# Kernel tuning notes

Measured on AMD Instinct MI355X. Metric: run time of the kernel, lower is better.

The kernel has to match this reference:

```python
import jax, jax.numpy as jnp
import numpy as np
from jax import lax

T, B, H = 8192, 16, 256
D0, D1, D2 = 64, 64, 128


def setup_inputs() -> dict:
    key = jax.random.key(0)
    ks = jax.random.split(key, 16)
    k = 1.0 / np.sqrt(H)  # torch LSTMCell default init scale

    def u(kk, shape):
        return jax.random.uniform(kk, shape, jnp.float32, -k, k)

    inp = {
        "x0": jax.random.normal(ks[0], (T, B, D0), jnp.float32),
        "x1": jax.random.normal(ks[1], (T // 2, B, D1), jnp.float32),
        "x2": jax.random.normal(ks[2], (T // 4, B, D2), jnp.float32),
    }
    # one LSTMCell per possible concatenated input size: a=256 (all), b=128 (two), c=64 (one)
    sizes = [("a", D0 + D1 + D2), ("b", D0 + D1), ("c", D0)]
    i = 3
    for name, s in sizes:
        inp[f"W_ih_{name}"] = u(ks[i], (4 * H, s)); i += 1
        inp[f"W_hh_{name}"] = u(ks[i], (4 * H, H)); i += 1
        inp[f"b_ih_{name}"] = u(ks[i], (4 * H,)); i += 1
        inp[f"b_hh_{name}"] = u(ks[i], (4 * H,)); i += 1
    return inp


def _cell(x, h, c, Wih, Whh, bih, bhh):
    # torch.nn.LSTMCell: gates = x W_ih^T + b_ih + h W_hh^T + b_hh; order i,f,g,o
    g = x @ Wih.T + bih + h @ Whh.T + bhh
    i, f, gg, o = jnp.split(g, 4, axis=-1)
    c2 = jax.nn.sigmoid(f) * c + jax.nn.sigmoid(i) * jnp.tanh(gg)
    h2 = jax.nn.sigmoid(o) * jnp.tanh(c2)
    return h2, c2


def reference(x0, x1, x2,
              W_ih_a, W_hh_a, b_ih_a, b_hh_a,
              W_ih_b, W_hh_b, b_ih_b, b_hh_b,
              W_ih_c, W_hh_c, b_ih_c, b_hh_c):
    # ratios = [1, 2, 4]; active sets are nested: t%4==0 -> all 3, t%2==0 -> first 2, else first only
    def step(carry, t):
        h, c = carry

        def br_all(_):
            xt = jnp.concatenate([x0[t], x1[t // 2], x2[t // 4]], axis=-1)  # [B, 256]
            return _cell(xt, h, c, W_ih_a, W_hh_a, b_ih_a, b_hh_a)

        def br_two(_):
            xt = jnp.concatenate([x0[t], x1[t // 2]], axis=-1)  # [B, 128]
            return _cell(xt, h, c, W_ih_b, W_hh_b, b_ih_b, b_hh_b)

        def br_one(_):
            return _cell(x0[t], h, c, W_ih_c, W_hh_c, b_ih_c, b_hh_c)  # [B, 64]

        branch = jnp.where(t % 4 == 0, 0, jnp.where(t % 2 == 0, 1, 2))
        h2, c2 = lax.switch(branch, [br_all, br_two, br_one], None)
        return (h2, c2), h2

    h0 = jnp.zeros((B, H), jnp.float32)
    (_, _), ys = lax.scan(step, (h0, h0), jnp.arange(T))
    return ys  # [T, B, H]
```

## Files before the change

### kernel.cpp

```cpp
#include <hip/hip_runtime.h>
#include <stdint.h>


typedef _Float16 half8 __attribute__((ext_vector_type(8)));
typedef float floatx4 __attribute__((ext_vector_type(4)));
typedef unsigned int u32x4 __attribute__((ext_vector_type(4)));

#define T_STEPS 8192
#define NWG 16

__device__ __forceinline__ float fsig(float x) {
    return __builtin_amdgcn_rcpf(1.0f + __expf(-x));
}
__device__ __forceinline__ float ftanh(float x) {
    return 1.0f - 2.0f * __builtin_amdgcn_rcpf(1.0f + __expf(2.0f * x));
}

__device__ __forceinline__ half8 ld8w(const float* p) {
    floatx4 a = *(const floatx4*)p;
    floatx4 b = *(const floatx4*)(p + 4);
    half8 h;
    h[0] = (_Float16)a[0]; h[1] = (_Float16)a[1]; h[2] = (_Float16)a[2]; h[3] = (_Float16)a[3];
    h[4] = (_Float16)b[0]; h[5] = (_Float16)b[1]; h[6] = (_Float16)b[2]; h[7] = (_Float16)b[3];
    return h;
}

__device__ __forceinline__ void ld64_sc1(const void* p, u32x4& a, u32x4& b, u32x4& c, u32x4& d) {
    asm volatile(
        "global_load_dwordx4 %0, %4, off sc1\n\t"
        "global_load_dwordx4 %1, %4, off offset:16 sc1\n\t"
        "global_load_dwordx4 %2, %4, off offset:32 sc1\n\t"
        "global_load_dwordx4 %3, %4, off offset:48 sc1\n\t"
        "s_waitcnt vmcnt(0)"
        : "=&v"(a), "=&v"(b), "=&v"(c), "=&v"(d)
        : "v"(p)
        : "memory");
}
__device__ __forceinline__ void st16_sc1(void* p, u32x4 v) {
    asm volatile("global_store_dwordx4 %0, %1, off sc1" :: "v"(p), "v"(v) : "memory");
}

__global__ __launch_bounds__(256, 1) void lstm_kernel(
    const float* __restrict__ x0, const float* __restrict__ x1, const float* __restrict__ x2,
    const float* __restrict__ Wih_a, const float* __restrict__ Whh_a,
    const float* __restrict__ bih_a, const float* __restrict__ bhh_a,
    const float* __restrict__ Wih_b, const float* __restrict__ Whh_b,
    const float* __restrict__ bih_b, const float* __restrict__ bhh_b,
    const float* __restrict__ Wih_c, const float* __restrict__ Whh_c,
    const float* __restrict__ bih_c, const float* __restrict__ bhh_c,
    float* __restrict__ out, uint8_t* __restrict__ ws, int smask)
{
    const int tid = threadIdx.x;
    const int g   = blockIdx.x;
    const int w   = tid >> 6;
    const int l   = tid & 63;
    const int n   = l & 15;
    const int mg  = l >> 4;
    const int up  = n & 3;
    const int gt  = n >> 2;
    const int unit = g * 16 + w * 4 + up;
    const int R    = gt * 256 + unit;

    uint8_t* hring = ws;

    __shared__ _Float16 XH[16][520];

    half8 wfa[16], wfb[12], wfc[10];
    {
        const int ko = mg * 8;
        #pragma unroll
        for (int kt = 0; kt < 8; ++kt) wfa[kt]     = ld8w(Wih_a + (size_t)R * 256 + kt * 32 + ko);
        #pragma unroll
        for (int kt = 0; kt < 8; ++kt) wfa[8 + kt] = ld8w(Whh_a + (size_t)R * 256 + kt * 32 + ko);
        #pragma unroll
        for (int kt = 0; kt < 4; ++kt) wfb[kt]     = ld8w(Wih_b + (size_t)R * 128 + kt * 32 + ko);
        #pragma unroll
        for (int kt = 0; kt < 8; ++kt) wfb[4 + kt] = ld8w(Whh_b + (size_t)R * 256 + kt * 32 + ko);
        #pragma unroll
        for (int kt = 0; kt < 2; ++kt) wfc[kt]     = ld8w(Wih_c + (size_t)R * 64  + kt * 32 + ko);
        #pragma unroll
        for (int kt = 0; kt < 8; ++kt) wfc[2 + kt] = ld8w(Whh_c + (size_t)R * 256 + kt * 32 + ko);
    }
    const float ba = bih_a[R] + bhh_a[R];
    const float bb = bih_b[R] + bhh_b[R];
    const float bc = bih_c[R] + bhh_c[R];

    float cst[4] = {0.f, 0.f, 0.f, 0.f};

    for (int t = 0; t < T_STEPS; ++t) {
        __syncthreads();

        const int br = ((t & 3) == 0) ? 0 : (((t & 1) == 0) ? 1 : 2);
        const int kx = (br == 0) ? 256 : ((br == 1) ? 128 : 64);

        if (tid < 128) {
            const int m = tid >> 3, cg = (tid & 7) * 8;
            *(half8*)&XH[m][cg] = ld8w(x0 + (size_t)t * 1024 + m * 64 + cg);
        } else if (br < 2) {
            const int tt = tid - 128;
            const int m = tt >> 3, cg = (tt & 7) * 8;
            *(half8*)&XH[m][64 + cg] = ld8w(x1 + (size_t)(t >> 1) * 1024 + m * 64 + cg);
        }
        if (br == 0) {
            const int m = tid >> 4, cg = (tid & 15) * 8;
            *(half8*)&XH[m][128 + cg] = ld8w(x2 + (size_t)(t >> 2) * 2048 + m * 128 + cg);
        }

        {
            const int row = tid >> 4, u = tid & 15;
            _Float16* dst = &XH[row][kx + u * 16];
            if (t == 0) {
                *(u32x4*)dst       = (u32x4)0u;
                *(u32x4*)(dst + 8) = (u32x4)0u;
            } else {
                const uint32_t want = (uint32_t)(t - 1);
                const uint8_t* src = hring + (size_t)((t - 1) & smask) * 16384
                                   + (size_t)row * 1024 + (size_t)u * 64;
                u32x4 a, b, c, d;
                for (;;) {
                    ld64_sc1(src, a, b, c, d);
                    if (a[1] == want && a[3] == want && b[1] == want && b[3] == want &&
                        c[1] == want && c[3] == want && d[1] == want && d[3] == want)
                        break;
                }
                u32x4 lo = {a[0], a[2], b[0], b[2]};
                u32x4 hi = {c[0], c[2], d[0], d[2]};
                *(u32x4*)dst       = lo;
                *(u32x4*)(dst + 8) = hi;
            }
        }
        __syncthreads();

        floatx4 ac0 = {0.f, 0.f, 0.f, 0.f}, ac1 = {0.f, 0.f, 0.f, 0.f};
        {
            const int ao = mg * 8;
            if (br == 0) {
                #pragma unroll
                for (int kt = 0; kt < 16; kt += 2) {
                    ac0 = __builtin_amdgcn_mfma_f32_16x16x32_f16(
                        *(const half8*)&XH[n][kt * 32 + ao], wfa[kt], ac0, 0, 0, 0);
                    ac1 = __builtin_amdgcn_mfma_f32_16x16x32_f16(
                        *(const half8*)&XH[n][(kt + 1) * 32 + ao], wfa[kt + 1], ac1, 0, 0, 0);
                }
            } else if (br == 1) {
                #pragma unroll
                for (int kt = 0; kt < 12; kt += 2) {
                    ac0 = __builtin_amdgcn_mfma_f32_16x16x32_f16(
                        *(const half8*)&XH[n][kt * 32 + ao], wfb[kt], ac0, 0, 0, 0);
                    ac1 = __builtin_amdgcn_mfma_f32_16x16x32_f16(
                        *(const half8*)&XH[n][(kt + 1) * 32 + ao], wfb[kt + 1], ac1, 0, 0, 0);
                }
            } else {
                #pragma unroll
                for (int kt = 0; kt < 10; kt += 2) {
                    ac0 = __builtin_amdgcn_mfma_f32_16x16x32_f16(
                        *(const half8*)&XH[n][kt * 32 + ao], wfc[kt], ac0, 0, 0, 0);
                    ac1 = __builtin_amdgcn_mfma_f32_16x16x32_f16(
                        *(const half8*)&XH[n][(kt + 1) * 32 + ao], wfc[kt + 1], ac1, 0, 0, 0);
                }
            }
        }
        const floatx4 acc = ac0 + ac1;

        const float bsel = (br == 0) ? ba : ((br == 1) ? bb : bc);
        float tv[4];
        #pragma unroll
        for (int r = 0; r < 4; ++r) {
            const float gv = acc[r] + bsel;
            tv[r] = (gt == 2) ? ftanh(gv) : fsig(gv);
        }
        float h2v[4];
        const int b0 = l & ~12;
        #pragma unroll
        for (int r = 0; r < 4; ++r) {
            const float vi = __shfl(tv[r], b0,      64);
            const float vf = __shfl(tv[r], b0 + 4,  64);
            const float vg = __shfl(tv[r], b0 + 8,  64);
            const float vo = __shfl(tv[r], b0 + 12, 64);
            const float c2 = vf * cst[r] + vi * vg;
            cst[r] = c2;
            h2v[r] = vo * ftanh(c2);
        }

        {
            uint8_t* sb = hring + (size_t)(t & smask) * 16384 + (size_t)(8 * g + 2 * w) * 8;
            const int s0 = l & ~15;
            #pragma unroll
            for (int r = 0; r < 4; ++r) {
                const unsigned hv =
                    (unsigned)__builtin_bit_cast(unsigned short, (_Float16)h2v[r]);
                const unsigned v0 = (unsigned)__shfl((int)hv, s0,     64);
                const unsigned v1 = (unsigned)__shfl((int)hv, s0 + 1, 64);
                const unsigned v2 = (unsigned)__shfl((int)hv, s0 + 2, 64);
                const unsigned v3 = (unsigned)__shfl((int)hv, s0 + 3, 64);
                if (n == 0) {
                    u32x4 pk = { (v0 & 0xffffu) | (v1 << 16), (unsigned)t,
                                 (v2 & 0xffffu) | (v3 << 16), (unsigned)t };
                    st16_sc1(sb + (size_t)(mg * 4 + r) * 1024, pk);
                }
            }
        }

        if (gt == 0) {
            float* op = out + (size_t)t * 4096 + (size_t)(mg * 4) * 256 + unit;
            #pragma unroll
            for (int r = 0; r < 4; ++r) op[r * 256] = h2v[r];
        }
    }
}

extern "C" void kernel_launch(void* const* d_in, const int* in_sizes, int n_in,
                              void* d_out, int out_size, void* d_ws, size_t ws_size,
                              hipStream_t stream) {
    (void)in_sizes; (void)n_in; (void)out_size;
    const int smask = (ws_size >= 4 * 16384) ? 3 : 1;
    hipLaunchKernelGGL(lstm_kernel, dim3(NWG), dim3(256), 0, stream,
        (const float*)d_in[0], (const float*)d_in[1], (const float*)d_in[2],
        (const float*)d_in[3], (const float*)d_in[4], (const float*)d_in[5], (const float*)d_in[6],
        (const float*)d_in[7], (const float*)d_in[8], (const float*)d_in[9], (const float*)d_in[10],
        (const float*)d_in[11], (const float*)d_in[12], (const float*)d_in[13], (const float*)d_in[14],
        (float*)d_out, (uint8_t*)d_ws, smask);
}
```

Before: 19.66 ms.

## Co-locate workgroups on one XCD and exchange hidden state through a local-cache ring

```diff
diff --git a/kernel.cpp b/kernel.cpp
--- a/kernel.cpp
+++ b/kernel.cpp
@@ -7,7 +7,7 @@
 typedef unsigned int u32x4 __attribute__((ext_vector_type(4)));
 
 #define T_STEPS 8192
-#define NWG 16
+#define FASTN 4096
 
 __device__ __forceinline__ float fsig(float x) {
     return __builtin_amdgcn_rcpf(1.0f + __expf(-x));
@@ -25,6 +25,20 @@
     return h;
 }
 
+__device__ __forceinline__ void ld64_sc0(const void* p, u32x4& a, u32x4& b, u32x4& c, u32x4& d) {
+    asm volatile(
+        "global_load_dwordx4 %0, %4, off sc0\n\t"
+        "global_load_dwordx4 %1, %4, off offset:16 sc0\n\t"
+        "global_load_dwordx4 %2, %4, off offset:32 sc0\n\t"
+        "global_load_dwordx4 %3, %4, off offset:48 sc0\n\t"
+        "s_waitcnt vmcnt(0)"
+        : "=&v"(a), "=&v"(b), "=&v"(c), "=&v"(d)
+        : "v"(p)
+        : "memory");
+}
+__device__ __forceinline__ void st16_sc0(void* p, u32x4 v) {
+    asm volatile("global_store_dwordx4 %0, %1, off sc0" :: "v"(p), "v"(v) : "memory");
+}
 __device__ __forceinline__ void ld64_sc1(const void* p, u32x4& a, u32x4& b, u32x4& c, u32x4& d) {
     asm volatile(
         "global_load_dwordx4 %0, %4, off sc1\n\t"
@@ -40,6 +54,12 @@
     asm volatile("global_store_dwordx4 %0, %1, off sc1" :: "v"(p), "v"(v) : "memory");
 }
 
+__device__ __forceinline__ bool tags_ok(const u32x4& a, const u32x4& b,
+                                        const u32x4& c, const u32x4& d, uint32_t want) {
+    return a[1] == want && a[3] == want && b[1] == want && b[3] == want &&
+           c[1] == want && c[3] == want && d[1] == want && d[3] == want;
+}
+
 __global__ __launch_bounds__(256, 1) void lstm_kernel(
     const float* __restrict__ x0, const float* __restrict__ x1, const float* __restrict__ x2,
     const float* __restrict__ Wih_a, const float* __restrict__ Whh_a,
@@ -48,10 +68,35 @@
     const float* __restrict__ bih_b, const float* __restrict__ bhh_b,
     const float* __restrict__ Wih_c, const float* __restrict__ Whh_c,
     const float* __restrict__ bih_c, const float* __restrict__ bhh_c,
-    float* __restrict__ out, uint8_t* __restrict__ ws, int smask)
+    float* __restrict__ out, uint8_t* __restrict__ safering, uint8_t* __restrict__ fastring,
+    uint32_t* __restrict__ cnt, int smaskS, int smaskF, int mode)
 {
     const int tid = threadIdx.x;
-    const int g   = blockIdx.x;
+
+    __shared__ int s_g;
+    if (tid == 0) {
+        int gg;
+        if (mode != 0) {
+            uint32_t xcc;
+            asm volatile("s_getreg_b32 %0, hwreg(20, 0, 32)" : "=s"(xcc));
+            xcc &= 7u;
+            const uint32_t my = atomicAdd(&cnt[xcc], 1u);
+            if (my == 15u) atomicCAS(&cnt[8], 0u, xcc + 1u);
+            uint32_t ch;
+            while ((ch = __hip_atomic_load(&cnt[8], __ATOMIC_RELAXED,
+                                           __HIP_MEMORY_SCOPE_AGENT)) == 0u) {
+                __builtin_amdgcn_s_sleep(8);
+            }
+            gg = (ch == xcc + 1u && my < 16u) ? (int)my : -1;
+        } else {
+            gg = (blockIdx.x < 16) ? (int)blockIdx.x : -1;
+        }
+        s_g = gg;
+    }
+    __syncthreads();
+    const int g = s_g;
+    if (g < 0) return;
+
     const int w   = tid >> 6;
     const int l   = tid & 63;
     const int n   = l & 15;
@@ -61,8 +106,6 @@
     const int unit = g * 16 + w * 4 + up;
     const int R    = gt * 256 + unit;
 
-    uint8_t* hring = ws;
-
     __shared__ _Float16 XH[16][520];
 
     half8 wfa[16], wfb[12], wfc[10];
@@ -86,6 +129,7 @@
     const float bc = bih_c[R] + bhh_c[R];
 
     float cst[4] = {0.f, 0.f, 0.f, 0.f};
+    int useFast = (mode != 0);
 
     for (int t = 0; t < T_STEPS; ++t) {
         __syncthreads();
@@ -113,15 +157,24 @@
                 *(u32x4*)dst       = (u32x4)0u;
                 *(u32x4*)(dst + 8) = (u32x4)0u;
             } else {
-                const uint32_t want = (uint32_t)(t - 1);
-                const uint8_t* src = hring + (size_t)((t - 1) & smask) * 16384
-                                   + (size_t)row * 1024 + (size_t)u * 64;
+                const uint32_t want = (uint32_t)t;
+                const size_t off = (size_t)row * 1024 + (size_t)u * 64;
                 u32x4 a, b, c, d;
-                for (;;) {
-                    ld64_sc1(src, a, b, c, d);
-                    if (a[1] == want && a[3] == want && b[1] == want && b[3] == want &&
-                        c[1] == want && c[3] == want && d[1] == want && d[3] == want)
-                        break;
+                bool got = false;
+                if (useFast) {
+                    const uint8_t* srcF = fastring + (size_t)((t - 1) & smaskF) * 16384 + off;
+                    for (int i = 0; i < FASTN; ++i) {
+                        ld64_sc0(srcF, a, b, c, d);
+                        if (tags_ok(a, b, c, d, want)) { got = true; break; }
+                    }
+                    if (!got) useFast = 0;
+                }
+                if (!got) {
+                    const uint8_t* srcS = safering + (size_t)((t - 1) & smaskS) * 16384 + off;
+                    for (;;) {
+                        ld64_sc1(srcS, a, b, c, d);
+                        if (tags_ok(a, b, c, d, want)) break;
+                    }
                 }
                 u32x4 lo = {a[0], a[2], b[0], b[2]};
                 u32x4 hi = {c[0], c[2], d[0], d[2]};
@@ -183,7 +236,9 @@
         }
 
         {
-            uint8_t* sb = hring + (size_t)(t & smask) * 16384 + (size_t)(8 * g + 2 * w) * 8;
+            const size_t colb = (size_t)(8 * g + 2 * w) * 8;
+            uint8_t* sbS = safering + (size_t)(t & smaskS) * 16384 + colb;
+            uint8_t* sbF = fastring + (size_t)(t & smaskF) * 16384 + colb;
             const int s0 = l & ~15;
             #pragma unroll
             for (int r = 0; r < 4; ++r) {
@@ -194,9 +249,10 @@
                 const unsigned v2 = (unsigned)__shfl((int)hv, s0 + 2, 64);
                 const unsigned v3 = (unsigned)__shfl((int)hv, s0 + 3, 64);
                 if (n == 0) {
-                    u32x4 pk = { (v0 & 0xffffu) | (v1 << 16), (unsigned)t,
-                                 (v2 & 0xffffu) | (v3 << 16), (unsigned)t };
-                    st16_sc1(sb + (size_t)(mg * 4 + r) * 1024, pk);
+                    u32x4 pk = { (v0 & 0xffffu) | (v1 << 16), (unsigned)(t + 1),
+                                 (v2 & 0xffffu) | (v3 << 16), (unsigned)(t + 1) };
+                    if (mode != 0) st16_sc0(sbF + (size_t)(mg * 4 + r) * 1024, pk);
+                    st16_sc1(sbS + (size_t)(mg * 4 + r) * 1024, pk);
                 }
             }
         }
@@ -213,11 +269,25 @@
                               void* d_out, int out_size, void* d_ws, size_t ws_size,
                               hipStream_t stream) {
     (void)in_sizes; (void)n_in; (void)out_size;
-    const int smask = (ws_size >= 4 * 16384) ? 3 : 1;
-    hipLaunchKernelGGL(lstm_kernel, dim3(NWG), dim3(256), 0, stream,
+    uint8_t* ws = (uint8_t*)d_ws;
+    int mode, smaskS, smaskF;
+    size_t fast_off, cnt_off;
+    if (ws_size >= (size_t)8 * 16384 + 64) {
+        mode = 1; smaskS = 3; smaskF = 3; fast_off = 4 * 16384; cnt_off = 8 * 16384;
+    } else if (ws_size >= (size_t)4 * 16384 + 64) {
+        mode = 1; smaskS = 1; smaskF = 1; fast_off = 2 * 16384; cnt_off = 4 * 16384;
+    } else {
+        mode = 0; smaskS = (ws_size >= (size_t)4 * 16384) ? 3 : 1; smaskF = smaskS;
+        fast_off = 0; cnt_off = 0;
+    }
+    if (mode != 0) {
+        hipMemsetAsync(ws + cnt_off, 0, 64, stream);
+    }
+    hipLaunchKernelGGL(lstm_kernel, dim3(256), dim3(256), 0, stream,
         (const float*)d_in[0], (const float*)d_in[1], (const float*)d_in[2],
         (const float*)d_in[3], (const float*)d_in[4], (const float*)d_in[5], (const float*)d_in[6],
         (const float*)d_in[7], (const float*)d_in[8], (const float*)d_in[9], (const float*)d_in[10],
         (const float*)d_in[11], (const float*)d_in[12], (const float*)d_in[13], (const float*)d_in[14],
-        (float*)d_out, (uint8_t*)d_ws, smask);
-}
+        (float*)d_out, ws, ws + fast_off,
+        (uint32_t*)(ws + cnt_off), smaskS, smaskF, mode);
+}
```

After: 27.50 ms. 1.4x slower.

## Prefetch inputs two steps ahead and overlap input GEMM with h wait

Applied to the files above, without the earlier changes.

```diff
diff --git a/kernel.cpp b/kernel.cpp
--- a/kernel.cpp
+++ b/kernel.cpp
@@ -16,13 +16,16 @@
     return 1.0f - 2.0f * __builtin_amdgcn_rcpf(1.0f + __expf(2.0f * x));
 }
 
-__device__ __forceinline__ half8 ld8w(const float* p) {
-    floatx4 a = *(const floatx4*)p;
-    floatx4 b = *(const floatx4*)(p + 4);
+__device__ __forceinline__ half8 cvt8(floatx4 a, floatx4 b) {
     half8 h;
     h[0] = (_Float16)a[0]; h[1] = (_Float16)a[1]; h[2] = (_Float16)a[2]; h[3] = (_Float16)a[3];
     h[4] = (_Float16)b[0]; h[5] = (_Float16)b[1]; h[6] = (_Float16)b[2]; h[7] = (_Float16)b[3];
     return h;
+}
+__device__ __forceinline__ half8 ld8w(const float* p) {
+    floatx4 a = *(const floatx4*)p;
+    floatx4 b = *(const floatx4*)(p + 4);
+    return cvt8(a, b);
 }
 
 __device__ __forceinline__ void ld64_sc1(const void* p, u32x4& a, u32x4& b, u32x4& c, u32x4& d) {
@@ -63,7 +66,8 @@
 
     uint8_t* hring = ws;
 
-    __shared__ _Float16 XH[16][520];
+    __shared__ _Float16 XB[2][16][264];
+    __shared__ _Float16 HB[16][264];
 
     half8 wfa[16], wfb[12], wfc[10];
     {
@@ -85,35 +89,85 @@
     const float bb = bih_b[R] + bhh_b[R];
     const float bc = bih_c[R] + bhh_c[R];
 
+    const int pm  = (tid & 127) >> 3;
+    const int pcg = (tid & 7) * 8;
+    const int qm  = tid >> 4;
+    const int qcg = (tid & 15) * 8;
+
+    floatx4 z4 = {0.f, 0.f, 0.f, 0.f};
+    floatx4 a0A = z4, a1A = z4, b0A = z4, b1A = z4;
+    floatx4 a0B = z4, a1B = z4, b0B = z4, b1B = z4;
+
+    auto issue = [&](int ts, floatx4& A0, floatx4& A1, floatx4& B0, floatx4& B1) {
+        const int brn = ((ts & 3) == 0) ? 0 : (((ts & 1) == 0) ? 1 : 2);
+        if (tid < 128) {
+            const floatx4* s = (const floatx4*)(x0 + (size_t)ts * 1024 + pm * 64 + pcg);
+            A0 = s[0]; A1 = s[1];
+        } else if (brn < 2) {
+            const floatx4* s = (const floatx4*)(x1 + (size_t)(ts >> 1) * 1024 + pm * 64 + pcg);
+            A0 = s[0]; A1 = s[1];
+        }
+        if (brn == 0) {
+            const floatx4* s = (const floatx4*)(x2 + (size_t)(ts >> 2) * 2048 + qm * 128 + qcg);
+            B0 = s[0]; B1 = s[1];
+        }
+    };
+    auto stage = [&](int ts, floatx4 A0, floatx4 A1, floatx4 B0, floatx4 B1) {
+        const int brn = ((ts & 3) == 0) ? 0 : (((ts & 1) == 0) ? 1 : 2);
+        const int xb  = ts & 1;
+        if (tid < 128)     *(half8*)&XB[xb][pm][pcg]       = cvt8(A0, A1);
+        else if (brn < 2)  *(half8*)&XB[xb][pm][64 + pcg]  = cvt8(A0, A1);
+        if (brn == 0)      *(half8*)&XB[xb][qm][128 + qcg] = cvt8(B0, B1);
+    };
+
+    {
+        floatx4 A0 = z4, A1 = z4, B0 = z4, B1 = z4;
+        issue(0, A0, A1, B0, B1);
+        stage(0, A0, A1, B0, B1);
+    }
+    issue(1, a0B, a1B, b0B, b1B);
+
     float cst[4] = {0.f, 0.f, 0.f, 0.f};
 
     for (int t = 0; t < T_STEPS; ++t) {
         __syncthreads();
 
         const int br = ((t & 3) == 0) ? 0 : (((t & 1) == 0) ? 1 : 2);
-        const int kx = (br == 0) ? 256 : ((br == 1) ? 128 : 64);
-
-        if (tid < 128) {
-            const int m = tid >> 3, cg = (tid & 7) * 8;
-            *(half8*)&XH[m][cg] = ld8w(x0 + (size_t)t * 1024 + m * 64 + cg);
-        } else if (br < 2) {
-            const int tt = tid - 128;
-            const int m = tt >> 3, cg = (tt & 7) * 8;
-            *(half8*)&XH[m][64 + cg] = ld8w(x1 + (size_t)(t >> 1) * 1024 + m * 64 + cg);
-        }
+        const int ao = mg * 8;
+        const int xb = t & 1;
+
+        floatx4 ac0 = {0.f, 0.f, 0.f, 0.f}, ac1 = {0.f, 0.f, 0.f, 0.f};
         if (br == 0) {
-            const int m = tid >> 4, cg = (tid & 15) * 8;
-            *(half8*)&XH[m][128 + cg] = ld8w(x2 + (size_t)(t >> 2) * 2048 + m * 128 + cg);
+            #pragma unroll
+            for (int kt = 0; kt < 8; kt += 2) {
+                ac0 = __builtin_amdgcn_mfma_f32_16x16x32_f16(
+                    *(const half8*)&XB[xb][n][kt * 32 + ao], wfa[kt], ac0, 0, 0, 0);
+                ac1 = __builtin_amdgcn_mfma_f32_16x16x32_f16(
+                    *(const half8*)&XB[xb][n][(kt + 1) * 32 + ao], wfa[kt + 1], ac1, 0, 0, 0);
+            }
+        } else if (br == 1) {
+            #pragma unroll
+            for (int kt = 0; kt < 4; kt += 2) {
+                ac0 = __builtin_amdgcn_mfma_f32_16x16x32_f16(
+                    *(const half8*)&XB[xb][n][kt * 32 + ao], wfb[kt], ac0, 0, 0, 0);
+                ac1 = __builtin_amdgcn_mfma_f32_16x16x32_f16(
+                    *(const half8*)&XB[xb][n][(kt + 1) * 32 + ao], wfb[kt + 1], ac1, 0, 0, 0);
+            }
+        } else {
+            ac0 = __builtin_amdgcn_mfma_f32_16x16x32_f16(
+                *(const half8*)&XB[xb][n][ao], wfc[0], ac0, 0, 0, 0);
+            ac1 = __builtin_amdgcn_mfma_f32_16x16x32_f16(
+                *(const half8*)&XB[xb][n][32 + ao], wfc[1], ac1, 0, 0, 0);
         }
 
         {
             const int row = tid >> 4, u = tid & 15;
-            _Float16* dst = &XH[row][kx + u * 16];
+            _Float16* dst = &HB[row][u * 16];
             if (t == 0) {
                 *(u32x4*)dst       = (u32x4)0u;
                 *(u32x4*)(dst + 8) = (u32x4)0u;
             } else {
-                const uint32_t want = (uint32_t)(t - 1);
+                const uint32_t want = (uint32_t)t;
                 const uint8_t* src = hring + (size_t)((t - 1) & smask) * 16384
                                    + (size_t)row * 1024 + (size_t)u * 64;
                 u32x4 a, b, c, d;
@@ -129,35 +183,37 @@
                 *(u32x4*)(dst + 8) = hi;
             }
         }
+
+        if (t + 2 < T_STEPS) {
+            if ((t & 1) == 0) issue(t + 2, a0A, a1A, b0A, b1A);
+            else              issue(t + 2, a0B, a1B, b0B, b1B);
+        }
+
         __syncthreads();
 
-        floatx4 ac0 = {0.f, 0.f, 0.f, 0.f}, ac1 = {0.f, 0.f, 0.f, 0.f};
-        {
-            const int ao = mg * 8;
-            if (br == 0) {
-                #pragma unroll
-                for (int kt = 0; kt < 16; kt += 2) {
-                    ac0 = __builtin_amdgcn_mfma_f32_16x16x32_f16(
-                        *(const half8*)&XH[n][kt * 32 + ao], wfa[kt], ac0, 0, 0, 0);
-                    ac1 = __builtin_amdgcn_mfma_f32_16x16x32_f16(
-                        *(const half8*)&XH[n][(kt + 1) * 32 + ao], wfa[kt + 1], ac1, 0, 0, 0);
-                }
-            } else if (br == 1) {
-                #pragma unroll
-                for (int kt = 0; kt < 12; kt += 2) {
-                    ac0 = __builtin_amdgcn_mfma_f32_16x16x32_f16(
-                        *(const half8*)&XH[n][kt * 32 + ao], wfb[kt], ac0, 0, 0, 0);
-                    ac1 = __builtin_amdgcn_mfma_f32_16x16x32_f16(
-                        *(const half8*)&XH[n][(kt + 1) * 32 + ao], wfb[kt + 1], ac1, 0, 0, 0);
-                }
-            } else {
-                #pragma unroll
-                for (int kt = 0; kt < 10; kt += 2) {
-                    ac0 = __builtin_amdgcn_mfma_f32_16x16x32_f16(
-                        *(const half8*)&XH[n][kt * 32 + ao], wfc[kt], ac0, 0, 0, 0);
-                    ac1 = __builtin_amdgcn_mfma_f32_16x16x32_f16(
-                        *(const half8*)&XH[n][(kt + 1) * 32 + ao], wfc[kt + 1], ac1, 0, 0, 0);
-                }
+        if (br == 0) {
+            #pragma unroll
+            for (int kt = 0; kt < 8; kt += 2) {
+                ac0 = __builtin_amdgcn_mfma_f32_16x16x32_f16(
+                    *(const half8*)&HB[n][kt * 32 + ao], wfa[8 + kt], ac0, 0, 0, 0);
+                ac1 = __builtin_amdgcn_mfma_f32_16x16x32_f16(
+                    *(const half8*)&HB[n][(kt + 1) * 32 + ao], wfa[9 + kt], ac1, 0, 0, 0);
+            }
+        } else if (br == 1) {
+            #pragma unroll
+            for (int kt = 0; kt < 8; kt += 2) {
+                ac0 = __builtin_amdgcn_mfma_f32_16x16x32_f16(
+                    *(const half8*)&HB[n][kt * 32 + ao], wfb[4 + kt], ac0, 0, 0, 0);
+                ac1 = __builtin_amdgcn_mfma_f32_16x16x32_f16(
+                    *(const half8*)&HB[n][(kt + 1) * 32 + ao], wfb[5 + kt], ac1, 0, 0, 0);
+            }
+        } else {
+            #pragma unroll
+            for (int kt = 0; kt < 8; kt += 2) {
+                ac0 = __builtin_amdgcn_mfma_f32_16x16x32_f16(
+                    *(const half8*)&HB[n][kt * 32 + ao], wfc[2 + kt], ac0, 0, 0, 0);
+                ac1 = __builtin_amdgcn_mfma_f32_16x16x32_f16(
+                    *(const half8*)&HB[n][(kt + 1) * 32 + ao], wfc[3 + kt], ac1, 0, 0, 0);
             }
         }
         const floatx4 acc = ac0 + ac1;
@@ -194,8 +250,8 @@
                 const unsigned v2 = (unsigned)__shfl((int)hv, s0 + 2, 64);
                 const unsigned v3 = (unsigned)__shfl((int)hv, s0 + 3, 64);
                 if (n == 0) {
-                    u32x4 pk = { (v0 & 0xffffu) | (v1 << 16), (unsigned)t,
-                                 (v2 & 0xffffu) | (v3 << 16), (unsigned)t };
+                    u32x4 pk = { (v0 & 0xffffu) | (v1 << 16), (unsigned)(t + 1),
+                                 (v2 & 0xffffu) | (v3 << 16), (unsigned)(t + 1) };
                     st16_sc1(sb + (size_t)(mg * 4 + r) * 1024, pk);
                 }
             }
@@ -205,6 +261,11 @@
             float* op = out + (size_t)t * 4096 + (size_t)(mg * 4) * 256 + unit;
             #pragma unroll
             for (int r = 0; r < 4; ++r) op[r * 256] = h2v[r];
+        }
+
+        if (t + 1 < T_STEPS) {
+            if (t & 1) stage(t + 1, a0A, a1A, b0A, b1A);
+            else       stage(t + 1, a0B, a1B, b0B, b1B);
         }
     }
 }
```

Measured after the change: 20.01 ms. Within noise of the previous version (+1.8%).
